# Kernel tuning notes

Measured on AMD Instinct MI355X. Metric: run time of the kernel, lower is better.

## Reference

```python
import jax, jax.numpy as jnp
import numpy as np

B, F, D, K = 4096, 1, 256, 65536

def setup_inputs() -> dict:
    key = jax.random.key(0)
    k1, k2, k3 = jax.random.split(key, 3)
    xhat_BFD = jax.random.normal(k1, (B, F, D), dtype=jnp.float32)
    x_BD = jax.random.normal(k2, (B * F, D), dtype=jnp.float32)
    centroids = jax.random.normal(k3, (K, D), dtype=jnp.float32)
    return {"xhat_BFD": xhat_BFD, "x_BD": x_BD, "centroids": centroids}

def reference(xhat_BFD, x_BD, centroids):
    c_sq_K = jnp.sum(centroids * centroids, axis=-1)            # [K]
    dists_BK = c_sq_K[None, :] - 2.0 * (x_BD @ centroids.T)     # [B*F, K] (GEMM-based distances)
    codes_B = jnp.argmin(dists_BK, axis=-1)                      # [B*F]
    quant_x_BD = centroids[codes_B]                              # embedding lookup of winners
    Bb, Ff, Dd = xhat_BFD.shape
    xhat_next = quant_x_BD.reshape(Bb, Ff, Dd)
    codes_BF = codes_B.reshape(Bb, Ff)
    return xhat_next, codes_BF
```

## Files before the change

kernel.cpp:

```cpp
#include <hip/hip_runtime.h>
#include <hip/hip_bf16.h>
#include <math.h>


#define DDIM 256
#define QTILE 128
#define STSZ 8192
#define QCAP 48
#define F16_MINN 6.103515625e-5f

typedef __attribute__((ext_vector_type(8))) _Float16 half8;
typedef __attribute__((ext_vector_type(4))) _Float16 half4;
typedef __attribute__((ext_vector_type(4))) float f32x4;

__device__ __forceinline__ void gl_lds16(const void* g, void* l) {
  __builtin_amdgcn_global_load_lds((const __attribute__((address_space(1))) void*)g,
                                   (__attribute__((address_space(3))) void*)l, 16, 0, 0);
}

__device__ __forceinline__ unsigned fkey(float d) {
  unsigned ud = __float_as_uint(d);
  return ud ^ (((int)ud < 0) ? 0xFFFFFFFFu : 0x80000000u);
}

__global__ __launch_bounds__(256) void splitc_kernel(const float* __restrict__ in,
                                                     _Float16* __restrict__ o0,
                                                     float* __restrict__ c_sq) {
  int i = blockIdx.x * 256 + threadIdx.x;
  int lane = (int)threadIdx.x & 63;
  float4 v = ((const float4*)in)[i];
  float vv[4] = {v.x, v.y, v.z, v.w};
  half4 h0;
#pragma unroll
  for (int e = 0; e < 4; ++e)
    h0[e] = (fabsf(vv[e]) < F16_MINN) ? (_Float16)0.f : (_Float16)vv[e];
  *(half4*)(o0 + (size_t)i * 4) = h0;
  float s = fmaf(v.x, v.x, fmaf(v.y, v.y, fmaf(v.z, v.z, v.w * v.w)));
#pragma unroll
  for (int off = 32; off > 0; off >>= 1) s += __shfl_down(s, off, 64);
  if (lane == 0) c_sq[i >> 6] = s;
}

__global__ __launch_bounds__(256) void splitx_kernel(const float* __restrict__ in,
                                                     _Float16* __restrict__ o0, int n4,
                                                     unsigned* __restrict__ ctl) {
  if (blockIdx.x == 0 && threadIdx.x < 64) ctl[threadIdx.x] = 0u;
  int i = blockIdx.x * 256 + threadIdx.x;
  if (i >= n4) return;
  float4 v = ((const float4*)in)[i];
  float vv[4] = {v.x, v.y, v.z, v.w};
  half4 h0;
#pragma unroll
  for (int e = 0; e < 4; ++e)
    h0[e] = (fabsf(vv[e]) < F16_MINN) ? (_Float16)0.f : (_Float16)vv[e];
  *(half4*)(o0 + (size_t)i * 4) = h0;
}

__global__ __launch_bounds__(256) void cmax_kernel(const float* __restrict__ c_sq,
                                                   unsigned* __restrict__ ctl) {
  __shared__ float red[4];
  int t = blockIdx.x * 256 + (int)threadIdx.x;
  float4 v = ((const float4*)c_sq)[t];
  float m = fmaxf(fmaxf(v.x, v.y), fmaxf(v.z, v.w));
#pragma unroll
  for (int off = 32; off > 0; off >>= 1) m = fmaxf(m, __shfl_down(m, off, 64));
  int lane = (int)threadIdx.x & 63, w = (int)threadIdx.x >> 6;
  if (lane == 0) red[w] = m;
  __syncthreads();
  if (threadIdx.x == 0) {
    m = fmaxf(fmaxf(red[0], red[1]), fmaxf(red[2], red[3]));
    atomicMax(&ctl[32], __float_as_uint(m));
  }
}

__global__ __launch_bounds__(1024) void scan_kernel(
    const _Float16* __restrict__ x0, const _Float16* __restrict__ c0,
    const float* __restrict__ c_sq, float* __restrict__ dm,
    float* __restrict__ pm) {
  __shared__ __align__(16) _Float16 As0[32768];
  __shared__ float pmred[2048];

  const int kc = blockIdx.x, qb = blockIdx.y;
  const int tid = (int)threadIdx.x;
  const int lane = tid & 63, w = tid >> 6;
  const int col = lane & 15, quad = lane >> 4;
  const int qrow0 = qb * QTILE;

  pmred[tid] = INFINITY;
  pmred[tid + 1024] = INFINITY;

#pragma unroll
  for (int i = 0; i < 4; ++i) {
    int u = i * 1024 + tid;
    int q = u & 127, s = u >> 7;
    gl_lds16(x0 + (size_t)(qrow0 + q) * DDIM + s * 8, As0 + (size_t)u * 8);
  }
  __syncthreads();

  for (int ct = 0; ct < STSZ / 512; ++ct) {
    const int cbase = kc * STSZ + ct * 512 + w * 32;
    f32x4 acc[2][8];
#pragma unroll
    for (int cm = 0; cm < 2; ++cm)
#pragma unroll
      for (int qn = 0; qn < 8; ++qn) acc[cm][qn] = (f32x4)0.0f;

#pragma unroll 2
    for (int kt = 0; kt < 8; ++kt) {
      const int k0 = kt * 32;
      half8 cf[2];
#pragma unroll
      for (int cm = 0; cm < 2; ++cm)
        cf[cm] = *(const half8*)(c0 + (size_t)(cbase + cm * 16 + col) * DDIM + k0 + quad * 8);
#pragma unroll
      for (int qn = 0; qn < 8; ++qn) {
        half8 qf = *(const half8*)(As0 + (size_t)(((kt * 4 + quad) * QTILE) + qn * 16 + col) * 8);
#pragma unroll
        for (int cm = 0; cm < 2; ++cm)
          acc[cm][qn] = __builtin_amdgcn_mfma_f32_16x16x32_f16(cf[cm], qf, acc[cm][qn], 0, 0, 0);
      }
    }

    f32x4 csv[2];
#pragma unroll
    for (int cm = 0; cm < 2; ++cm)
      csv[cm] = *(const f32x4*)(c_sq + cbase + cm * 16 + quad * 4);
    const int grp = kc * (STSZ / 32) + ct * 16 + w;
    float* dmg = dm + (size_t)grp * 4096 + qrow0;
#pragma unroll
    for (int qn = 0; qn < 8; ++qn) {
      float mq = INFINITY;
#pragma unroll
      for (int cm = 0; cm < 2; ++cm)
#pragma unroll
        for (int rg = 0; rg < 4; ++rg)
          mq = fminf(mq, fmaf(-2.0f, acc[cm][qn][rg], csv[cm][rg]));
      mq = fminf(mq, __shfl_xor(mq, 16, 64));
      mq = fminf(mq, __shfl_xor(mq, 32, 64));
      if (quad == 0) {
        dmg[qn * 16 + col] = mq;
        const int pi = w * 128 + qn * 16 + col;
        pmred[pi] = fminf(pmred[pi], mq);
      }
    }
  }

  __syncthreads();
  if (tid < 128) {
    float m = INFINITY;
#pragma unroll
    for (int i = 0; i < 16; ++i) m = fminf(m, pmred[i * 128 + tid]);
    pm[(size_t)kc * 4096 + qrow0 + tid] = m;
  }
}

__global__ __launch_bounds__(512) void finish_kernel(
    const float* __restrict__ pm, const float* __restrict__ x,
    const unsigned* __restrict__ ctl, const float* __restrict__ dm,
    const float* __restrict__ cent, const float* __restrict__ c_sq,
    float* __restrict__ out) {
  __shared__ float Tl[16];
  __shared__ unsigned cnt16[16];
  __shared__ unsigned short candL[16][QCAP];
  __shared__ float xred[16][33];
  __shared__ unsigned long long bestL[16];

  const int t = (int)threadIdx.x;
  const int w = t >> 6, lane = t & 63;
  const int q0 = (int)blockIdx.x * 16;

  {
    int qi = t >> 5, ch = t & 31;
    const float4* xr = (const float4*)(x + (size_t)(q0 + qi) * DDIM + ch * 8);
    float s = 0.f;
#pragma unroll
    for (int j = 0; j < 2; ++j) {
      float4 v = xr[j];
      s = fmaf(v.x, v.x, fmaf(v.y, v.y, fmaf(v.z, v.z, fmaf(v.w, v.w, s))));
    }
    xred[qi][ch] = s;
    if (t < 16) cnt16[t] = 0u;
  }
  __syncthreads();
  if (t < 16) {
    float xsq = 0.f;
#pragma unroll
    for (int i = 0; i < 32; ++i) xsq += xred[t][i];
    float M = INFINITY;
#pragma unroll
    for (int i = 0; i < 8; ++i) M = fminf(M, pm[i * 4096 + q0 + t]);
    float cmaxsq = __uint_as_float(ctl[32]);
    Tl[t] = M + 0.0078125f * sqrtf(xsq * cmaxsq) + 1.0f;
  }
  __syncthreads();

  {
    const int qi = t & 15, g0 = t >> 4;
    const float Tq = Tl[qi];
#pragma unroll 4
    for (int i = 0; i < 64; ++i) {
      int g = g0 + i * 32;
      float v = dm[(size_t)g * 4096 + q0 + qi];
      if (v <= Tq) {
        unsigned slot = atomicAdd(&cnt16[qi], 1u);
        if (slot < QCAP) candL[qi][slot] = (unsigned short)g;
      }
    }
  }
  __syncthreads();

#pragma unroll
  for (int k = 0; k < 2; ++k) {
    const int qi = w + k * 8;
    const unsigned n = cnt16[qi];
    unsigned long long bq = 0xFFFFFFFFFFFFFFFFull;
    if (n >= 1 && n <= QCAP) {
      int dh = (lane & 1) * 128;
      const float4* xr = (const float4*)(x + (size_t)(q0 + qi) * DDIM + dh);
      for (unsigned sl = 0; sl < n; ++sl) {
        int g = (int)candL[qi][sl];
        int c = g * 32 + (lane >> 1);
        const float4* cr = (const float4*)(cent + (size_t)c * DDIM + dh);
        float s = 0.f;
#pragma unroll
        for (int i = 0; i < 32; ++i) {
          float4 a = xr[i], bb = cr[i];
          s = fmaf(a.x, bb.x, fmaf(a.y, bb.y, fmaf(a.z, bb.z, fmaf(a.w, bb.w, s))));
        }
        s += __shfl_xor(s, 1, 64);
        float d = (lane & 1) ? INFINITY : fmaf(-2.0f, s, c_sq[c]);
        unsigned long long pkv = ((unsigned long long)fkey(d) << 32) | (unsigned)c;
        if (pkv < bq) bq = pkv;
      }
    } else {
      const float4* xr = (const float4*)(x + (size_t)(q0 + qi) * DDIM);
      for (int c = lane; c < 65536; c += 64) {
        const float4* cr = (const float4*)(cent + (size_t)c * DDIM);
        float s = 0.f;
#pragma unroll 16
        for (int i = 0; i < 64; ++i) {
          float4 a = xr[i], bb = cr[i];
          s = fmaf(a.x, bb.x, fmaf(a.y, bb.y, fmaf(a.z, bb.z, fmaf(a.w, bb.w, s))));
        }
        float d = fmaf(-2.0f, s, c_sq[c]);
        unsigned long long pkv = ((unsigned long long)fkey(d) << 32) | (unsigned)c;
        if (pkv < bq) bq = pkv;
      }
    }
#pragma unroll
    for (int off = 1; off < 64; off <<= 1) {
      unsigned long long o = __shfl_xor(bq, off, 64);
      if (o < bq) bq = o;
    }
    if (lane == 0) bestL[qi] = bq;
  }
  __syncthreads();

  {
    int qi = t >> 5, part = t & 31;
    int idx = (int)(unsigned)(bestL[qi] & 0xFFFFFFFFu);
    const float4* cr = (const float4*)(cent + (size_t)idx * DDIM);
    float4* orow = (float4*)(out + (size_t)(q0 + qi) * DDIM);
#pragma unroll
    for (int j = 0; j < 2; ++j) orow[part * 2 + j] = cr[part * 2 + j];
    if (part == 0) out[(size_t)4096 * DDIM + q0 + qi] = (float)idx;
  }
}

extern "C" void kernel_launch(void* const* d_in, const int* in_sizes, int n_in,
                              void* d_out, int out_size, void* d_ws, size_t ws_size,
                              hipStream_t stream) {
  const float* x    = (const float*)d_in[1];
  const float* cent = (const float*)d_in[2];
  float* out = (float*)d_out;
  char* ws = (char*)d_ws;

  const size_t OFF_C0   = 0;
  const size_t OFF_X0   = 33554432;
  const size_t OFF_CSQ  = 35651584;
  const size_t OFF_CTL  = 35913728;
  const size_t OFF_DM   = 35913984;
  const size_t OFF_PM   = 69468416;
  const size_t NEED     = 72089600;
  if (ws_size < NEED) return;

  _Float16* c0 = (_Float16*)(ws + OFF_C0);
  _Float16* x0 = (_Float16*)(ws + OFF_X0);
  float* c_sq = (float*)(ws + OFF_CSQ);
  unsigned* ctl = (unsigned*)(ws + OFF_CTL);
  float* dm = (float*)(ws + OFF_DM);
  float* pm = (float*)(ws + OFF_PM);

  splitc_kernel<<<16384, 256, 0, stream>>>(cent, c0, c_sq);
  splitx_kernel<<<1024, 256, 0, stream>>>(x, x0, 4096 * 256 / 4, ctl);
  cmax_kernel<<<64, 256, 0, stream>>>(c_sq, ctl);
  scan_kernel<<<dim3(8, 32), 1024, 0, stream>>>(x0, c0, c_sq, dm, pm);
  finish_kernel<<<256, 512, 0, stream>>>(pm, x, ctl, dm, cent, c_sq, out);
}
```

Baseline: 326.1 us.

## Split scan blocks across centroid halves and fuse cmax into splitc

The scan kernel drops from 1024-thread blocks to 512-thread blocks, with each block covering half of each 512-centroid tile. That doubles the grid to 512 blocks, and launch bounds (512,4) allow more blocks per CU for better occupancy and load balance. Partial minima now come in 16 slices per query, and finish reads all 16. Separately, the centroid-norm max is folded into splitc via a block reduction plus atomicMax, and ctl is reset with a memset, which removes the cmax kernel launch. In exchange, the query tile is loaded into LDS twice as often and there are 16384 atomics instead of 64.

```diff
diff --git a/kernel.cpp b/kernel.cpp
--- a/kernel.cpp
+++ b/kernel.cpp
@@ -25,9 +25,11 @@
 
 __global__ __launch_bounds__(256) void splitc_kernel(const float* __restrict__ in,
                                                      _Float16* __restrict__ o0,
-                                                     float* __restrict__ c_sq) {
+                                                     float* __restrict__ c_sq,
+                                                     unsigned* __restrict__ ctl) {
+  __shared__ float red[4];
   int i = blockIdx.x * 256 + threadIdx.x;
-  int lane = (int)threadIdx.x & 63;
+  int lane = (int)threadIdx.x & 63, w = (int)threadIdx.x >> 6;
   float4 v = ((const float4*)in)[i];
   float vv[4] = {v.x, v.y, v.z, v.w};
   half4 h0;
@@ -38,13 +40,16 @@
   float s = fmaf(v.x, v.x, fmaf(v.y, v.y, fmaf(v.z, v.z, v.w * v.w)));
 #pragma unroll
   for (int off = 32; off > 0; off >>= 1) s += __shfl_down(s, off, 64);
-  if (lane == 0) c_sq[i >> 6] = s;
+  if (lane == 0) { c_sq[i >> 6] = s; red[w] = s; }
+  __syncthreads();
+  if (threadIdx.x == 0) {
+    float m = fmaxf(fmaxf(red[0], red[1]), fmaxf(red[2], red[3]));
+    atomicMax(&ctl[32], __float_as_uint(m));
+  }
 }
 
 __global__ __launch_bounds__(256) void splitx_kernel(const float* __restrict__ in,
-                                                     _Float16* __restrict__ o0, int n4,
-                                                     unsigned* __restrict__ ctl) {
-  if (blockIdx.x == 0 && threadIdx.x < 64) ctl[threadIdx.x] = 0u;
+                                                     _Float16* __restrict__ o0, int n4) {
   int i = blockIdx.x * 256 + threadIdx.x;
   if (i >= n4) return;
   float4 v = ((const float4*)in)[i];
@@ -56,49 +61,33 @@
   *(half4*)(o0 + (size_t)i * 4) = h0;
 }
 
-__global__ __launch_bounds__(256) void cmax_kernel(const float* __restrict__ c_sq,
-                                                   unsigned* __restrict__ ctl) {
-  __shared__ float red[4];
-  int t = blockIdx.x * 256 + (int)threadIdx.x;
-  float4 v = ((const float4*)c_sq)[t];
-  float m = fmaxf(fmaxf(v.x, v.y), fmaxf(v.z, v.w));
-#pragma unroll
-  for (int off = 32; off > 0; off >>= 1) m = fmaxf(m, __shfl_down(m, off, 64));
-  int lane = (int)threadIdx.x & 63, w = (int)threadIdx.x >> 6;
-  if (lane == 0) red[w] = m;
-  __syncthreads();
-  if (threadIdx.x == 0) {
-    m = fmaxf(fmaxf(red[0], red[1]), fmaxf(red[2], red[3]));
-    atomicMax(&ctl[32], __float_as_uint(m));
-  }
-}
-
-__global__ __launch_bounds__(1024) void scan_kernel(
+__global__ __launch_bounds__(512, 4) void scan_kernel(
     const _Float16* __restrict__ x0, const _Float16* __restrict__ c0,
     const float* __restrict__ c_sq, float* __restrict__ dm,
     float* __restrict__ pm) {
   __shared__ __align__(16) _Float16 As0[32768];
-  __shared__ float pmred[2048];
-
-  const int kc = blockIdx.x, qb = blockIdx.y;
+  __shared__ float pmred[1024];
+
+  const int kc = blockIdx.x;
+  const int qb = (int)blockIdx.y >> 1, chalf = (int)blockIdx.y & 1;
   const int tid = (int)threadIdx.x;
   const int lane = tid & 63, w = tid >> 6;
   const int col = lane & 15, quad = lane >> 4;
   const int qrow0 = qb * QTILE;
 
   pmred[tid] = INFINITY;
-  pmred[tid + 1024] = INFINITY;
-
-#pragma unroll
-  for (int i = 0; i < 4; ++i) {
-    int u = i * 1024 + tid;
+  pmred[tid + 512] = INFINITY;
+
+#pragma unroll
+  for (int i = 0; i < 8; ++i) {
+    int u = i * 512 + tid;
     int q = u & 127, s = u >> 7;
     gl_lds16(x0 + (size_t)(qrow0 + q) * DDIM + s * 8, As0 + (size_t)u * 8);
   }
   __syncthreads();
 
   for (int ct = 0; ct < STSZ / 512; ++ct) {
-    const int cbase = kc * STSZ + ct * 512 + w * 32;
+    const int cbase = kc * STSZ + ct * 512 + chalf * 256 + w * 32;
     f32x4 acc[2][8];
 #pragma unroll
     for (int cm = 0; cm < 2; ++cm)
@@ -125,7 +114,7 @@
 #pragma unroll
     for (int cm = 0; cm < 2; ++cm)
       csv[cm] = *(const f32x4*)(c_sq + cbase + cm * 16 + quad * 4);
-    const int grp = kc * (STSZ / 32) + ct * 16 + w;
+    const int grp = kc * (STSZ / 32) + ct * 16 + chalf * 8 + w;
     float* dmg = dm + (size_t)grp * 4096 + qrow0;
 #pragma unroll
     for (int qn = 0; qn < 8; ++qn) {
@@ -149,8 +138,8 @@
   if (tid < 128) {
     float m = INFINITY;
 #pragma unroll
-    for (int i = 0; i < 16; ++i) m = fminf(m, pmred[i * 128 + tid]);
-    pm[(size_t)kc * 4096 + qrow0 + tid] = m;
+    for (int i = 0; i < 8; ++i) m = fminf(m, pmred[i * 128 + tid]);
+    pm[(size_t)(kc * 2 + chalf) * 4096 + qrow0 + tid] = m;
   }
 }
 
@@ -188,7 +177,7 @@
     for (int i = 0; i < 32; ++i) xsq += xred[t][i];
     float M = INFINITY;
 #pragma unroll
-    for (int i = 0; i < 8; ++i) M = fminf(M, pm[i * 4096 + q0 + t]);
+    for (int i = 0; i < 16; ++i) M = fminf(M, pm[i * 4096 + q0 + t]);
     float cmaxsq = __uint_as_float(ctl[32]);
     Tl[t] = M + 0.0078125f * sqrtf(xsq * cmaxsq) + 1.0f;
   }
@@ -291,9 +280,9 @@
   float* dm = (float*)(ws + OFF_DM);
   float* pm = (float*)(ws + OFF_PM);
 
-  splitc_kernel<<<16384, 256, 0, stream>>>(cent, c0, c_sq);
-  splitx_kernel<<<1024, 256, 0, stream>>>(x, x0, 4096 * 256 / 4, ctl);
-  cmax_kernel<<<64, 256, 0, stream>>>(c_sq, ctl);
-  scan_kernel<<<dim3(8, 32), 1024, 0, stream>>>(x0, c0, c_sq, dm, pm);
+  hipMemsetAsync(ctl, 0, 256, stream);
+  splitc_kernel<<<16384, 256, 0, stream>>>(cent, c0, c_sq, ctl);
+  splitx_kernel<<<1024, 256, 0, stream>>>(x, x0, 4096 * 256 / 4);
+  scan_kernel<<<dim3(8, 64), 512, 0, stream>>>(x0, c0, c_sq, dm, pm);
   finish_kernel<<<256, 512, 0, stream>>>(pm, x, ctl, dm, cent, c_sq, out);
 }
```

Result: slower. 498.1 us (+52.8%).
